# Kernel optimization log

Hardware: AMD Instinct MI355X
Metric: run time of the kernel (lower is better)

The kernel has to match this reference:

```python
import jax, jax.numpy as jnp
import numpy as np

N = 4096        # nodes
E = 131072      # edges (avg degree 32)
IN = 512        # in_channels
HID = 512       # hidden_channels
HEADS = 4       # GAT heads
LAYERS = 3      # residual GCN layers
G = 16          # graphs in batch
OUT = 1         # out_channels
NEG_SLOPE = 0.2 # GAT LeakyReLU slope


def setup_inputs() -> dict:
    key = jax.random.key(0)
    ks = jax.random.split(key, 9)
    s = 0.02
    x = jax.random.normal(ks[0], (N, IN), dtype=jnp.float32)
    edge_index = jax.random.randint(ks[1], (2, E), 0, N)
    batch = jnp.sort(jax.random.randint(ks[2], (N,), 0, G))
    W_gat = jax.random.normal(ks[3], (HEADS, IN, HID), dtype=jnp.float32) * s
    a_src = jax.random.normal(ks[4], (HEADS, HID), dtype=jnp.float32) * s
    a_dst = jax.random.normal(ks[5], (HEADS, HID), dtype=jnp.float32) * s
    W_gcn = jax.random.normal(ks[6], (LAYERS, HID, HID), dtype=jnp.float32) * s
    fc_w = jax.random.normal(ks[7], (HID, OUT), dtype=jnp.float32) * s
    fc_b = jnp.zeros((OUT,), dtype=jnp.float32)
    return {"x": x, "edge_index": edge_index, "batch": batch,
            "W_gat": W_gat, "a_src": a_src, "a_dst": a_dst,
            "W_gcn": W_gcn, "fc_w": fc_w, "fc_b": fc_b}


def reference(x, edge_index, batch, W_gat, a_src, a_dst, W_gcn, fc_w, fc_b):
    src, dst = edge_index[0], edge_index[1]

    # ---- LatentRelationCapturerGAT: multi-head GAT, one output per head ----
    h = jnp.einsum('nc,hcd->nhd', x, W_gat)                    # [N,H,D]
    lg_src = jnp.einsum('nhd,hd->nh', h, a_src)                # [N,H]
    lg_dst = jnp.einsum('nhd,hd->nh', h, a_dst)                # [N,H]
    e = jax.nn.leaky_relu(lg_src[src] + lg_dst[dst], NEG_SLOPE)  # [E,H]
    # segment softmax over incoming edges of each destination node
    m = jax.ops.segment_max(e, dst, num_segments=N)            # [N,H]
    w = jnp.exp(e - m[dst])                                    # [E,H]
    z = jax.ops.segment_sum(w, dst, num_segments=N)            # [N,H]
    alpha = w / (z[dst] + 1e-16)                               # [E,H]
    H0 = jax.ops.segment_sum(alpha[:, :, None] * h[src], dst, num_segments=N)  # [N,H,D]

    # ---- dense adjacency build + GCN normalization (shared across heads) ----
    A = jnp.zeros((N, N), dtype=x.dtype).at[src, dst].set(1.0)
    A = A + jnp.eye(N, dtype=x.dtype)                          # self-loops
    dinv = jax.lax.rsqrt(jnp.sum(A, axis=1))                   # deg >= 1
    A_hat = dinv[:, None] * A * dinv[None, :]                  # D^-1/2 (A+I) D^-1/2

    # ---- DeepResidualGCN: H <- relu(A_hat @ H @ W_l) + H (heads batched) ----
    H = H0
    for l in range(W_gcn.shape[0]):
        P = jnp.einsum('nm,mhd->nhd', A_hat, H)                # propagate
        H = jax.nn.relu(jnp.einsum('nhd,de->nhe', P, W_gcn[l])) + H

    # ---- per-head global mean pool, then mean over heads ----
    ones = jnp.ones((N,), dtype=x.dtype)
    cnt = jnp.maximum(jax.ops.segment_sum(ones, batch, num_segments=G), 1.0)  # [G]
    pooled = jax.ops.segment_sum(H, batch, num_segments=G) / cnt[:, None, None]  # [G,H,D]
    feats = pooled.mean(axis=1)                                # [G,D]

    return feats @ fc_w + fc_b                                 # [G,OUT]
```

## Files before the change

kernel.cpp:

```cpp
#include <hip/hip_runtime.h>
#include <cstdint>
#include <cstddef>

#define Nn    4096
#define Ee    131072
#define INC   512
#define HIDC  512
#define HEADS 4
#define NLAY  3
#define GG    16
#define FW    2048
#define ALDS  2112
#define BLDS  4160

typedef __attribute__((ext_vector_type(8))) short bfrag;
typedef __attribute__((ext_vector_type(4))) float ffrag;

__device__ __forceinline__ ushort f2bf(float v){
  uint u = __builtin_bit_cast(uint, v);
  u += 0x7fffu + ((u>>16)&1u);
  return (ushort)(u>>16);
}
__device__ __forceinline__ float bf2f(ushort s){
  uint u = ((uint)s)<<16; return __builtin_bit_cast(float, u);
}
__device__ __forceinline__ void fma8(float* acc, uint4 g, float w){
  uint u[4] = {g.x, g.y, g.z, g.w};
  #pragma unroll
  for (int q=0;q<4;q++){
    float lo = __builtin_bit_cast(float, u[q]<<16);
    float hi = __builtin_bit_cast(float, u[q] & 0xffff0000u);
    acc[2*q]   += w*lo;
    acc[2*q+1] += w*hi;
  }
}
__device__ __forceinline__ void pack8(void* p, const float* a){
  uint4 o;
  o.x = (uint)f2bf(a[0]) | ((uint)f2bf(a[1])<<16);
  o.y = (uint)f2bf(a[2]) | ((uint)f2bf(a[3])<<16);
  o.z = (uint)f2bf(a[4]) | ((uint)f2bf(a[5])<<16);
  o.w = (uint)f2bf(a[6]) | ((uint)f2bf(a[7])<<16);
  *(uint4*)p = o;
}

__global__ __launch_bounds__(256) void prep(
    const float* __restrict__ x, ushort* __restrict__ Xb,
    const float* __restrict__ Wgat, ushort* __restrict__ Tgat,
    const float* __restrict__ Wgcn, ushort* __restrict__ Tgcn,
    const int* __restrict__ src, const int* __restrict__ dst,
    int* __restrict__ indeg, unsigned int* __restrict__ bitmap,
    int* __restrict__ cnt_s, int* __restrict__ flag){
  __shared__ float tile[32][33];
  int b = blockIdx.x, t = threadIdx.x;
  if (b < 8192){
    int i = b*256 + t;
    Xb[i] = f2bf(x[i]);
  } else if (b < 9984){
    int idx = b - 8192;
    int z = idx >> 8, xy = idx & 255;
    const float* W; ushort* T; int bb;
    if (z < 4){ W = Wgat; T = Tgat; bb = z; } else { W = Wgcn; T = Tgcn; bb = z-4; }
    int r0 = (xy>>4)*32, c0 = (xy&15)*32;
    int i = t>>3, j0 = (t&7)*4;
    const float* Wb = W + (size_t)bb*512*512;
    float4 v = *(const float4*)(Wb + (size_t)(r0+i)*512 + c0 + j0);
    tile[i][j0]=v.x; tile[i][j0+1]=v.y; tile[i][j0+2]=v.z; tile[i][j0+3]=v.w;
    __syncthreads();
    ushort* o = T + (size_t)bb*512*512 + (size_t)(c0+i)*512 + r0 + j0;
    #pragma unroll
    for (int q=0;q<4;q++) o[q] = f2bf(tile[j0+q][i]);
  } else {
    int e = (b-9984)*256 + t; if (e>=Ee) return;
    int s = src[e], d = dst[e];
    atomicAdd(&indeg[d],1);
    unsigned int key = (unsigned int)s*Nn + (unsigned int)d;
    unsigned int bit = 1u<<(key&31);
    unsigned int old = atomicOr(&bitmap[key>>5], bit);
    int f = (old & bit) ? 0 : 1;
    flag[e] = f;
    if (f) atomicAdd(&cnt_s[s],1);
  }
}

__device__ __forceinline__ void gemm_core(
    const ushort* __restrict__ A, const ushort* __restrict__ B,
    const ushort* Res, ushort* Cb,
    int M, int N, int K, int relu_res, int m0, int n0,
    ushort* Ah, ushort* Bh)
{
  int t = threadIdx.x;
  int srA = t>>2, kqA = t&3;
  const ushort* pA = A + (size_t)(m0+srA)*K + kqA*8;
  int wA = (kqA*66 + srA)*8;
  int srB = t>>1, cB = t&1;
  const ushort* pB = B + (size_t)(n0+srB)*K + cB*16;
  int wB0 = ((2*cB)*130 + srB)*8;
  int wB1 = wB0 + 130*8;

  int wave = t>>6, lane = t&63;
  int wm = (wave&1)*32, wn = (wave>>1)*64;
  int lm = lane&15, quad = lane>>4;

  ffrag acc[2][4];
  #pragma unroll
  for (int i=0;i<2;i++){
    #pragma unroll
    for (int j=0;j<4;j++) acc[i][j] = (ffrag){0.f,0.f,0.f,0.f};
  }

  uint4 ra  = *(const uint4*)(pA);
  uint4 rb0 = *(const uint4*)(pB);  uint4 rb1 = *(const uint4*)(pB+8);
  *(uint4*)&Ah[wA]  = ra;
  *(uint4*)&Bh[wB0] = rb0; *(uint4*)&Bh[wB1] = rb1;
  if (K > 32){
    ra  = *(const uint4*)(pA+32);
    rb0 = *(const uint4*)(pB+32); rb1 = *(const uint4*)(pB+40);
  }
  __syncthreads();

  for (int k0 = 0; k0 < K; k0 += 32){
    int cur = (k0>>5)&1, nxt = cur^1;
    const ushort* Ac = Ah + cur*ALDS;
    const ushort* Bc = Bh + cur*BLDS;
    bfrag af[2];
    #pragma unroll
    for (int mt=0; mt<2; mt++)
      af[mt] = *(const bfrag*)&Ac[(quad*66 + wm + mt*16 + lm)*8];
    #pragma unroll
    for (int nt=0; nt<4; nt++){
      bfrag bf = *(const bfrag*)&Bc[(quad*130 + wn + nt*16 + lm)*8];
      #pragma unroll
      for (int mt=0; mt<2; mt++)
        acc[mt][nt] = __builtin_amdgcn_mfma_f32_16x16x32_bf16(af[mt], bf, acc[mt][nt], 0,0,0);
    }
    if (k0+32 < K){
      *(uint4*)&Ah[nxt*ALDS + wA]  = ra;
      *(uint4*)&Bh[nxt*BLDS + wB0] = rb0; *(uint4*)&Bh[nxt*BLDS + wB1] = rb1;
      if (k0+64 < K){
        ra  = *(const uint4*)(pA+k0+64);
        rb0 = *(const uint4*)(pB+k0+64); rb1 = *(const uint4*)(pB+k0+72);
      }
    }
    __syncthreads();
  }

  #pragma unroll
  for (int mt=0; mt<2; mt++){
    #pragma unroll
    for (int nt=0; nt<4; nt++){
      #pragma unroll
      for (int r=0;r<4;r++){
        int grow = m0 + wm + mt*16 + quad*4 + r;
        int gcol = n0 + wn + nt*16 + lm;
        size_t off = (size_t)grow*N + gcol;
        float v = acc[mt][nt][r];
        if (relu_res) v = fmaxf(v,0.f) + bf2f(Res[off]);
        Cb[off] = f2bf(v);
      }
    }
  }
}

__global__ __launch_bounds__(256) void gemm_bf(
    const ushort* __restrict__ A, const ushort* __restrict__ B,
    const ushort* Res, ushort* Cb,
    int M, int N, int K, int relu_res)
{
  __shared__ __align__(16) ushort Ah[2*ALDS];
  __shared__ __align__(16) ushort Bh[2*BLDS];
  gemm_core(A, B, Res, Cb, M, N, K, relu_res, blockIdx.y*64, blockIdx.x*128, Ah, Bh);
}

__global__ __launch_bounds__(256) void gat_gemm_ep2(
    const ushort* __restrict__ Xbf, const ushort* __restrict__ WgatT, ushort* __restrict__ hbf,
    const int* __restrict__ src, const int* __restrict__ dst, const int* __restrict__ flag,
    const int* __restrict__ rp_d, int* __restrict__ fill_d, int* __restrict__ slist,
    const int* __restrict__ rp_s, int* __restrict__ fill_s, int2* __restrict__ cw,
    const float* __restrict__ dinv)
{
  __shared__ __align__(16) ushort Ah[2*ALDS];
  __shared__ __align__(16) ushort Bh[2*BLDS];
  int b = blockIdx.x;
  if (b < 1024){
    int m0 = (b>>4)*64, n0 = (b&15)*128;
    gemm_core(Xbf, WgatT, nullptr, hbf, Nn, FW, INC, 0, m0, n0, Ah, Bh);
  } else {
    int e = (b-1024)*256 + threadIdx.x; if (e>=Ee) return;
    int s = src[e], d = dst[e];
    int p = atomicAdd(&fill_d[d],1); slist[rp_d[d]+p] = s;
    if (flag[e]){
      int q = atomicAdd(&fill_s[s],1);
      cw[rp_s[s]+q] = make_int2(d, __float_as_int(dinv[d]));
    }
  }
}

__global__ __launch_bounds__(256) void compute_lg(const ushort* __restrict__ hbf,
    const float* __restrict__ a_src, const float* __restrict__ a_dst,
    float* __restrict__ lgs, float* __restrict__ lgd){
  int n = blockIdx.x; int t = threadIdx.x;
  int hd = t>>6, lane = t&63;
  uint4 g = *(const uint4*)(hbf + (size_t)n*FW + hd*HIDC + lane*8);
  float h[8] = {0,0,0,0,0,0,0,0};
  fma8(h, g, 1.0f);
  float4 as0 = *(const float4*)(a_src + hd*HIDC + lane*8);
  float4 as1 = *(const float4*)(a_src + hd*HIDC + lane*8 + 4);
  float4 ad0 = *(const float4*)(a_dst + hd*HIDC + lane*8);
  float4 ad1 = *(const float4*)(a_dst + hd*HIDC + lane*8 + 4);
  float s1 = h[0]*as0.x + h[1]*as0.y + h[2]*as0.z + h[3]*as0.w
           + h[4]*as1.x + h[5]*as1.y + h[6]*as1.z + h[7]*as1.w;
  float s2 = h[0]*ad0.x + h[1]*ad0.y + h[2]*ad0.z + h[3]*ad0.w
           + h[4]*ad1.x + h[5]*ad1.y + h[6]*ad1.z + h[7]*ad1.w;
  for (int off=32; off; off>>=1){ s1 += __shfl_down(s1,off); s2 += __shfl_down(s2,off); }
  if (lane==0){ lgs[n*HEADS+hd]=s1; lgd[n*HEADS+hd]=s2; }
}

__global__ __launch_bounds__(1024) void scan3(const int* __restrict__ indeg, int* __restrict__ rp_d,
    const int* __restrict__ cnt_s, int* __restrict__ rp_s, float* __restrict__ dinv,
    const int* __restrict__ batch, int* __restrict__ goff){
  __shared__ int sums[1024];
  __shared__ int cnt2[GG];
  int t = threadIdx.x;
  if (blockIdx.x == 2){
    if (t<GG) cnt2[t]=0;
    __syncthreads();
    for (int i=t;i<Nn;i+=1024) atomicAdd(&cnt2[batch[i]],1);
    __syncthreads();
    if (t==0){ int run=0; for (int g=0; g<GG; g++){ goff[g]=run; run+=cnt2[g]; } goff[GG]=run; }
    return;
  }
  const int* cnt = blockIdx.x ? cnt_s : indeg;
  int* rowptr    = blockIdx.x ? rp_s  : rp_d;
  int v[4]; int s=0;
  #pragma unroll
  for (int i=0;i<4;i++){ int idx=t*4+i; v[i] = cnt[idx]; s+=v[i]; }
  sums[t]=s; __syncthreads();
  for (int off=1; off<1024; off<<=1){
    int other = (t>=off)? sums[t-off] : 0;
    __syncthreads();
    sums[t] += other;
    __syncthreads();
  }
  int run = (t>0)? sums[t-1] : 0;
  #pragma unroll
  for (int i=0;i<4;i++){
    int idx=t*4+i; rowptr[idx]=run; run+=v[i];
    if (blockIdx.x) dinv[idx] = 1.0f/sqrtf((float)(1+v[i]));
  }
  if (t==1023) rowptr[Nn]=sums[1023];
}

__global__ __launch_bounds__(256) void gat_aggregate(const ushort* __restrict__ hbf,
    const float* __restrict__ lgs, const float* __restrict__ lgd,
    const int* __restrict__ rowptr, const int* __restrict__ slist,
    ushort* __restrict__ Hbf){
  int t = threadIdx.x;
  int wv = __builtin_amdgcn_readfirstlane(t>>6);
  int lane = t&63;
  int b = blockIdx.x;
  int hd = __builtin_amdgcn_readfirstlane(b & 3);
  int n = ((b>>2)<<2) + wv;
  int beg = __builtin_amdgcn_readfirstlane(rowptr[n]);
  int end = __builtin_amdgcn_readfirstlane(rowptr[n+1]);
  int deg = end - beg;
  float ldst = lgd[n*HEADS+hd];
  float m_ = -3.4e38f, z_ = 0.f;
  for (int i=lane; i<deg; i+=64){
    int s = slist[beg+i];
    float v = lgs[s*HEADS+hd] + ldst;
    v = v>0.f ? v : 0.2f*v;
    float mn = fmaxf(m_, v);
    z_ = z_*__expf(m_-mn) + __expf(v-mn);
    m_ = mn;
  }
  for (int o=32;o;o>>=1){
    float mo = __shfl_down(m_,o), zo = __shfl_down(z_,o);
    float mn = fmaxf(m_, mo);
    z_ = z_*__expf(m_-mn) + zo*__expf(mo-mn);
    m_ = mn;
  }
  float mx = __shfl(m_,0);
  float zs = __shfl(z_,0);
  float inv = 1.f/(zs+1e-16f);
  float acc[8] = {0,0,0,0,0,0,0,0};
  const ushort* hb = hbf + hd*HIDC + lane*8;
  int i = beg;
  if (i+4 <= end){
    uint4 g0[4]; float lv0[4];
    #pragma unroll
    for (int q=0;q<4;q++){
      int s = slist[i+q];
      g0[q] = *(const uint4*)(hb + (size_t)s*FW);
      lv0[q] = lgs[s*HEADS+hd];
    }
    i += 4;
    for (; i+4<=end; i+=4){
      uint4 g1[4]; float lv1[4];
      #pragma unroll
      for (int q=0;q<4;q++){
        int s = slist[i+q];
        g1[q] = *(const uint4*)(hb + (size_t)s*FW);
        lv1[q] = lgs[s*HEADS+hd];
      }
      #pragma unroll
      for (int q=0;q<4;q++){
        float v = lv0[q] + ldst; v = v>0.f ? v : 0.2f*v;
        fma8(acc, g0[q], __expf(v-mx)*inv);
      }
      #pragma unroll
      for (int q=0;q<4;q++){ g0[q]=g1[q]; lv0[q]=lv1[q]; }
    }
    #pragma unroll
    for (int q=0;q<4;q++){
      float v = lv0[q] + ldst; v = v>0.f ? v : 0.2f*v;
      fma8(acc, g0[q], __expf(v-mx)*inv);
    }
  }
  for (; i<end; i++){
    int s = slist[i];
    uint4 g = *(const uint4*)(hb + (size_t)s*FW);
    float v = lgs[s*HEADS+hd] + ldst; v = v>0.f ? v : 0.2f*v;
    fma8(acc, g, __expf(v-mx)*inv);
  }
  size_t off = (size_t)n*FW + hd*HIDC + lane*8;
  pack8(Hbf + off, acc);
}

__global__ __launch_bounds__(256) void spmm_bf(const ushort* __restrict__ Hbf,
    ushort* __restrict__ Phi,
    const int* __restrict__ rowptr, const int2* __restrict__ cw, const float* __restrict__ dinv){
  int t = threadIdx.x;
  int wv = __builtin_amdgcn_readfirstlane(t>>6);
  int lane = t&63;
  int b = blockIdx.x;
  int ck = __builtin_amdgcn_readfirstlane(b & 3);
  int n = ((b>>2)<<2) + wv;
  int f = (ck<<9) + lane*8;
  float di = dinv[n];
  float acc[8] = {0,0,0,0,0,0,0,0};
  const ushort* hb = Hbf + f;
  uint4 self = *(const uint4*)(hb + (size_t)n*FW);
  fma8(acc, self, di*di);
  int beg = __builtin_amdgcn_readfirstlane(rowptr[n]);
  int end = __builtin_amdgcn_readfirstlane(rowptr[n+1]);
  int i = beg;
  if (i+4 <= end){
    int2 e0[4]; uint4 g0[4];
    #pragma unroll
    for (int q=0;q<4;q++) e0[q] = cw[i+q];
    #pragma unroll
    for (int q=0;q<4;q++) g0[q] = *(const uint4*)(hb + (size_t)e0[q].x*FW);
    i += 4;
    for (; i+4<=end; i+=4){
      int2 e1[4]; uint4 g1[4];
      #pragma unroll
      for (int q=0;q<4;q++) e1[q] = cw[i+q];
      #pragma unroll
      for (int q=0;q<4;q++) g1[q] = *(const uint4*)(hb + (size_t)e1[q].x*FW);
      #pragma unroll
      for (int q=0;q<4;q++) fma8(acc, g0[q], di*__int_as_float(e0[q].y));
      #pragma unroll
      for (int q=0;q<4;q++){ e0[q]=e1[q]; g0[q]=g1[q]; }
    }
    #pragma unroll
    for (int q=0;q<4;q++) fma8(acc, g0[q], di*__int_as_float(e0[q].y));
  }
  for (; i<end; i++){
    int2 e = cw[i];
    uint4 g = *(const uint4*)(hb + (size_t)e.x*FW);
    fma8(acc, g, di*__int_as_float(e.y));
  }
  pack8(Phi + (size_t)n*FW + f, acc);
}

__global__ __launch_bounds__(256) void pool_accum(const ushort* __restrict__ Hb,
    const int* __restrict__ batch, float* __restrict__ psum){
  int d2 = blockIdx.y*256 + threadIdx.x;
  int n0 = blockIdx.x*32;
  int g = batch[n0];
  float s0 = 0.f, s1 = 0.f;
  for (int k=0;k<32;k++){
    int n = n0+k;
    int gn = batch[n];
    if (gn != g){
      atomicAdd(&psum[(size_t)g*FW + d2*2],   s0);
      atomicAdd(&psum[(size_t)g*FW + d2*2+1], s1);
      s0=0.f; s1=0.f; g=gn;
    }
    uint v = *(const uint*)(Hb + (size_t)n*FW + d2*2);
    s0 += bf2f((ushort)(v&0xffff));
    s1 += bf2f((ushort)(v>>16));
  }
  atomicAdd(&psum[(size_t)g*FW + d2*2],   s0);
  atomicAdd(&psum[(size_t)g*FW + d2*2+1], s1);
}
__global__ __launch_bounds__(256) void final_out(const float* __restrict__ psum,
    const int* __restrict__ goff,
    const float* __restrict__ fc_w, const float* __restrict__ fc_b, float* __restrict__ out){
  int g = blockIdx.x; int t = threadIdx.x;
  float cinv = 0.25f / fmaxf((float)(goff[g+1]-goff[g]), 1.f);
  float p = 0.f;
  for (int d=t; d<HIDC; d+=256){
    float f = cinv*(psum[(size_t)g*FW+d] + psum[(size_t)g*FW+HIDC+d]
                  + psum[(size_t)g*FW+2*HIDC+d] + psum[(size_t)g*FW+3*HIDC+d]);
    p += f*fc_w[d];
  }
  __shared__ float red[4];
  for (int off=32; off; off>>=1) p += __shfl_down(p,off);
  if ((t&63)==0) red[t>>6]=p;
  __syncthreads();
  if (t==0) out[g] = red[0]+red[1]+red[2]+red[3] + fc_b[0];
}

extern "C" void kernel_launch(void* const* d_in, const int* in_sizes, int n_in,
                              void* d_out, int out_size, void* d_ws, size_t ws_size,
                              hipStream_t stream){
  const float* x      = (const float*)d_in[0];
  const int*   ei     = (const int*)d_in[1];
  const int*   batch  = (const int*)d_in[2];
  const float* W_gat  = (const float*)d_in[3];
  const float* a_src  = (const float*)d_in[4];
  const float* a_dst  = (const float*)d_in[5];
  const float* W_gcn  = (const float*)d_in[6];
  const float* fc_w   = (const float*)d_in[7];
  const float* fc_b   = (const float*)d_in[8];
  float* out = (float*)d_out;
  const int* src = ei;
  const int* dst = ei + Ee;

  char* w = (char*)d_ws;
  size_t off = 0;
  auto alloc = [&](size_t bytes)->char*{ char* p = w + off; off = (off + bytes + 255) & ~(size_t)255; return p; };
  ushort* hbf    = (ushort*)alloc((size_t)Nn*FW*2);
  ushort* Hbf    = (ushort*)alloc((size_t)Nn*FW*2);
  ushort* Xbf    = (ushort*)alloc((size_t)Nn*INC*2);
  ushort* WgatT  = (ushort*)alloc((size_t)HEADS*INC*HIDC*2);
  ushort* WgcnT  = (ushort*)alloc((size_t)NLAY*HIDC*HIDC*2);
  float* lgs    = (float*)alloc((size_t)Nn*HEADS*4);
  float* lgd    = (float*)alloc((size_t)Nn*HEADS*4);
  int* indeg    = (int*)alloc(Nn*4);
  int* fill_d   = (int*)alloc(Nn*4);
  int* cnt_s    = (int*)alloc(Nn*4);
  int* fill_s   = (int*)alloc(Nn*4);
  float* psum   = (float*)alloc((size_t)GG*FW*4);
  unsigned int* bitmap = (unsigned int*)alloc((size_t)Nn*Nn/8);
  size_t zero_bytes = (size_t)Nn*4*4 + (size_t)GG*FW*4 + (size_t)Nn*Nn/8;
  int* rowptr_d = (int*)alloc((Nn+1)*4);
  int* slist    = (int*)alloc(Ee*4);
  int* rowptr_s = (int*)alloc((Nn+1)*4);
  int2* cwlist  = (int2*)alloc((size_t)Ee*8);
  int* flag     = (int*)alloc(Ee*4);
  float* dinv   = (float*)alloc(Nn*4);
  int* goff     = (int*)alloc((GG+1)*4);
  ushort* Phi   = hbf;

  hipMemsetAsync(indeg, 0, zero_bytes, stream);

  prep<<<10496,256,0,stream>>>(x, Xbf, W_gat, WgatT, W_gcn, WgcnT,
                               src, dst, indeg, bitmap, cnt_s, flag);

  scan3<<<3,1024,0,stream>>>(indeg, rowptr_d, cnt_s, rowptr_s, dinv, batch, goff);

  gat_gemm_ep2<<<1536,256,0,stream>>>(Xbf, WgatT, hbf,
      src, dst, flag, rowptr_d, fill_d, slist, rowptr_s, fill_s, cwlist, dinv);

  compute_lg<<<Nn,256,0,stream>>>(hbf, a_src, a_dst, lgs, lgd);
  gat_aggregate<<<Nn,256,0,stream>>>(hbf, lgs, lgd, rowptr_d, slist, Hbf);

  for (int l=0;l<NLAY;l++){
    spmm_bf<<<Nn,256,0,stream>>>(Hbf, Phi, rowptr_s, cwlist, dinv);
    gemm_bf<<<dim3(HIDC/128, (Nn*HEADS)/64),256,0,stream>>>(Phi,
        WgcnT + (size_t)l*HIDC*HIDC,
        Hbf, Hbf, Nn*HEADS, HIDC, HIDC, 1);
  }

  pool_accum<<<dim3(Nn/32, FW/512),256,0,stream>>>(Hbf, batch, psum);
  final_out<<<GG,256,0,stream>>>(psum, goff, fc_w, fc_b, out);
}
```

Measured before the change: 361.5 us.

## Fuse x bf16 conversion into GAT GEMM loads and attention logits into epilogue

```diff
diff --git a/kernel.cpp b/kernel.cpp
--- a/kernel.cpp
+++ b/kernel.cpp
@@ -42,9 +42,16 @@
   o.w = (uint)f2bf(a[6]) | ((uint)f2bf(a[7])<<16);
   *(uint4*)p = o;
 }
+__device__ __forceinline__ uint4 cvt8(float4 a, float4 b){
+  uint4 o;
+  o.x = (uint)f2bf(a.x) | ((uint)f2bf(a.y)<<16);
+  o.y = (uint)f2bf(a.z) | ((uint)f2bf(a.w)<<16);
+  o.z = (uint)f2bf(b.x) | ((uint)f2bf(b.y)<<16);
+  o.w = (uint)f2bf(b.z) | ((uint)f2bf(b.w)<<16);
+  return o;
+}
 
 __global__ __launch_bounds__(256) void prep(
-    const float* __restrict__ x, ushort* __restrict__ Xb,
     const float* __restrict__ Wgat, ushort* __restrict__ Tgat,
     const float* __restrict__ Wgcn, ushort* __restrict__ Tgcn,
     const int* __restrict__ src, const int* __restrict__ dst,
@@ -52,12 +59,8 @@
     int* __restrict__ cnt_s, int* __restrict__ flag){
   __shared__ float tile[32][33];
   int b = blockIdx.x, t = threadIdx.x;
-  if (b < 8192){
-    int i = b*256 + t;
-    Xb[i] = f2bf(x[i]);
-  } else if (b < 9984){
-    int idx = b - 8192;
-    int z = idx >> 8, xy = idx & 255;
+  if (b < 1792){
+    int z = b >> 8, xy = b & 255;
     const float* W; ushort* T; int bb;
     if (z < 4){ W = Wgat; T = Tgat; bb = z; } else { W = Wgcn; T = Tgcn; bb = z-4; }
     int r0 = (xy>>4)*32, c0 = (xy&15)*32;
@@ -70,7 +73,7 @@
     #pragma unroll
     for (int q=0;q<4;q++) o[q] = f2bf(tile[j0+q][i]);
   } else {
-    int e = (b-9984)*256 + t; if (e>=Ee) return;
+    int e = (b-1792)*256 + t; if (e>=Ee) return;
     int s = src[e], d = dst[e];
     atomicAdd(&indeg[d],1);
     unsigned int key = (unsigned int)s*Nn + (unsigned int)d;
@@ -82,15 +85,17 @@
   }
 }
 
+template<bool AF32, bool FUSELG>
 __device__ __forceinline__ void gemm_core(
-    const ushort* __restrict__ A, const ushort* __restrict__ B,
+    const void* __restrict__ Av, const ushort* __restrict__ B,
     const ushort* Res, ushort* Cb,
-    int M, int N, int K, int relu_res, int m0, int n0,
-    ushort* Ah, ushort* Bh)
+    int N, int K, int relu_res, int m0, int n0,
+    ushort* Ah, ushort* Bh,
+    const float* a_src, const float* a_dst, float* lgs, float* lgd)
 {
+  __shared__ float lsum[64][2];
   int t = threadIdx.x;
   int srA = t>>2, kqA = t&3;
-  const ushort* pA = A + (size_t)(m0+srA)*K + kqA*8;
   int wA = (kqA*66 + srA)*8;
   int srB = t>>1, cB = t&1;
   const ushort* pB = B + (size_t)(n0+srB)*K + cB*16;
@@ -101,6 +106,10 @@
   int wm = (wave&1)*32, wn = (wave>>1)*64;
   int lm = lane&15, quad = lane>>4;
 
+  if (FUSELG){
+    if (t < 128) lsum[t>>1][t&1] = 0.f;
+  }
+
   ffrag acc[2][4];
   #pragma unroll
   for (int i=0;i<2;i++){
@@ -108,12 +117,18 @@
     for (int j=0;j<4;j++) acc[i][j] = (ffrag){0.f,0.f,0.f,0.f};
   }
 
-  uint4 ra  = *(const uint4*)(pA);
+  const ushort* pA16 = (const ushort*)Av + (size_t)(m0+srA)*K + kqA*8;
+  const float*  pA32 = (const float*)Av  + (size_t)(m0+srA)*K + kqA*8;
+
+  uint4 ra; float4 raf0, raf1;
+  if (AF32){ raf0 = *(const float4*)(pA32); raf1 = *(const float4*)(pA32+4); }
+  else     { ra = *(const uint4*)(pA16); }
   uint4 rb0 = *(const uint4*)(pB);  uint4 rb1 = *(const uint4*)(pB+8);
-  *(uint4*)&Ah[wA]  = ra;
+  *(uint4*)&Ah[wA]  = AF32 ? cvt8(raf0, raf1) : ra;
   *(uint4*)&Bh[wB0] = rb0; *(uint4*)&Bh[wB1] = rb1;
   if (K > 32){
-    ra  = *(const uint4*)(pA+32);
+    if (AF32){ raf0 = *(const float4*)(pA32+32); raf1 = *(const float4*)(pA32+36); }
+    else     { ra = *(const uint4*)(pA16+32); }
     rb0 = *(const uint4*)(pB+32); rb1 = *(const uint4*)(pB+40);
   }
   __syncthreads();
@@ -134,29 +149,53 @@
         acc[mt][nt] = __builtin_amdgcn_mfma_f32_16x16x32_bf16(af[mt], bf, acc[mt][nt], 0,0,0);
     }
     if (k0+32 < K){
-      *(uint4*)&Ah[nxt*ALDS + wA]  = ra;
+      *(uint4*)&Ah[nxt*ALDS + wA]  = AF32 ? cvt8(raf0, raf1) : ra;
       *(uint4*)&Bh[nxt*BLDS + wB0] = rb0; *(uint4*)&Bh[nxt*BLDS + wB1] = rb1;
       if (k0+64 < K){
-        ra  = *(const uint4*)(pA+k0+64);
+        if (AF32){ raf0 = *(const float4*)(pA32+k0+64); raf1 = *(const float4*)(pA32+k0+68); }
+        else     { ra = *(const uint4*)(pA16+k0+64); }
         rb0 = *(const uint4*)(pB+k0+64); rb1 = *(const uint4*)(pB+k0+72);
       }
     }
     __syncthreads();
   }
 
+  float asv[4], adv[4];
+  if (FUSELG){
+    #pragma unroll
+    for (int nt=0;nt<4;nt++){
+      int gcol = n0 + wn + nt*16 + lm;
+      asv[nt] = a_src[gcol]; adv[nt] = a_dst[gcol];
+    }
+  }
   #pragma unroll
   for (int mt=0; mt<2; mt++){
     #pragma unroll
-    for (int nt=0; nt<4; nt++){
-      #pragma unroll
-      for (int r=0;r<4;r++){
-        int grow = m0 + wm + mt*16 + quad*4 + r;
+    for (int r=0;r<4;r++){
+      int row = wm + mt*16 + quad*4 + r;
+      int grow = m0 + row;
+      float p1 = 0.f, p2 = 0.f;
+      #pragma unroll
+      for (int nt=0; nt<4; nt++){
         int gcol = n0 + wn + nt*16 + lm;
         size_t off = (size_t)grow*N + gcol;
         float v = acc[mt][nt][r];
         if (relu_res) v = fmaxf(v,0.f) + bf2f(Res[off]);
         Cb[off] = f2bf(v);
+        if (FUSELG){ p1 += v*asv[nt]; p2 += v*adv[nt]; }
       }
+      if (FUSELG){
+        atomicAdd(&lsum[row][0], p1);
+        atomicAdd(&lsum[row][1], p2);
+      }
+    }
+  }
+  if (FUSELG){
+    __syncthreads();
+    if (t < 64){
+      int hd = n0 >> 9;
+      atomicAdd(&lgs[(size_t)(m0+t)*HEADS + hd], lsum[t][0]);
+      atomicAdd(&lgd[(size_t)(m0+t)*HEADS + hd], lsum[t][1]);
     }
   }
 }
@@ -164,15 +203,19 @@
 __global__ __launch_bounds__(256) void gemm_bf(
     const ushort* __restrict__ A, const ushort* __restrict__ B,
     const ushort* Res, ushort* Cb,
-    int M, int N, int K, int relu_res)
+    int N, int K, int relu_res)
 {
   __shared__ __align__(16) ushort Ah[2*ALDS];
   __shared__ __align__(16) ushort Bh[2*BLDS];
-  gemm_core(A, B, Res, Cb, M, N, K, relu_res, blockIdx.y*64, blockIdx.x*128, Ah, Bh);
+  gemm_core<false,false>(A, B, Res, Cb, N, K, relu_res,
+                         blockIdx.y*64, blockIdx.x*128, Ah, Bh,
+                         nullptr, nullptr, nullptr, nullptr);
 }
 
 __global__ __launch_bounds__(256) void gat_gemm_ep2(
-    const ushort* __restrict__ Xbf, const ushort* __restrict__ WgatT, ushort* __restrict__ hbf,
+    const float* __restrict__ x, const ushort* __restrict__ WgatT, ushort* __restrict__ hbf,
+    const float* __restrict__ a_src, const float* __restrict__ a_dst,
+    float* __restrict__ lgs, float* __restrict__ lgd,
     const int* __restrict__ src, const int* __restrict__ dst, const int* __restrict__ flag,
     const int* __restrict__ rp_d, int* __restrict__ fill_d, int* __restrict__ slist,
     const int* __restrict__ rp_s, int* __restrict__ fill_s, int2* __restrict__ cw,
@@ -183,7 +226,8 @@
   int b = blockIdx.x;
   if (b < 1024){
     int m0 = (b>>4)*64, n0 = (b&15)*128;
-    gemm_core(Xbf, WgatT, nullptr, hbf, Nn, FW, INC, 0, m0, n0, Ah, Bh);
+    gemm_core<true,true>(x, WgatT, nullptr, hbf, FW, INC, 0, m0, n0, Ah, Bh,
+                         a_src, a_dst, lgs, lgd);
   } else {
     int e = (b-1024)*256 + threadIdx.x; if (e>=Ee) return;
     int s = src[e], d = dst[e];
@@ -193,26 +237,6 @@
       cw[rp_s[s]+q] = make_int2(d, __float_as_int(dinv[d]));
     }
   }
-}
-
-__global__ __launch_bounds__(256) void compute_lg(const ushort* __restrict__ hbf,
-    const float* __restrict__ a_src, const float* __restrict__ a_dst,
-    float* __restrict__ lgs, float* __restrict__ lgd){
-  int n = blockIdx.x; int t = threadIdx.x;
-  int hd = t>>6, lane = t&63;
-  uint4 g = *(const uint4*)(hbf + (size_t)n*FW + hd*HIDC + lane*8);
-  float h[8] = {0,0,0,0,0,0,0,0};
-  fma8(h, g, 1.0f);
-  float4 as0 = *(const float4*)(a_src + hd*HIDC + lane*8);
-  float4 as1 = *(const float4*)(a_src + hd*HIDC + lane*8 + 4);
-  float4 ad0 = *(const float4*)(a_dst + hd*HIDC + lane*8);
-  float4 ad1 = *(const float4*)(a_dst + hd*HIDC + lane*8 + 4);
-  float s1 = h[0]*as0.x + h[1]*as0.y + h[2]*as0.z + h[3]*as0.w
-           + h[4]*as1.x + h[5]*as1.y + h[6]*as1.z + h[7]*as1.w;
-  float s2 = h[0]*ad0.x + h[1]*ad0.y + h[2]*ad0.z + h[3]*ad0.w
-           + h[4]*ad1.x + h[5]*ad1.y + h[6]*ad1.z + h[7]*ad1.w;
-  for (int off=32; off; off>>=1){ s1 += __shfl_down(s1,off); s2 += __shfl_down(s2,off); }
-  if (lane==0){ lgs[n*HEADS+hd]=s1; lgd[n*HEADS+hd]=s2; }
 }
 
 __global__ __launch_bounds__(1024) void scan3(const int* __restrict__ indeg, int* __restrict__ rp_d,
@@ -433,18 +457,17 @@
   auto alloc = [&](size_t bytes)->char*{ char* p = w + off; off = (off + bytes + 255) & ~(size_t)255; return p; };
   ushort* hbf    = (ushort*)alloc((size_t)Nn*FW*2);
   ushort* Hbf    = (ushort*)alloc((size_t)Nn*FW*2);
-  ushort* Xbf    = (ushort*)alloc((size_t)Nn*INC*2);
   ushort* WgatT  = (ushort*)alloc((size_t)HEADS*INC*HIDC*2);
   ushort* WgcnT  = (ushort*)alloc((size_t)NLAY*HIDC*HIDC*2);
-  float* lgs    = (float*)alloc((size_t)Nn*HEADS*4);
-  float* lgd    = (float*)alloc((size_t)Nn*HEADS*4);
   int* indeg    = (int*)alloc(Nn*4);
   int* fill_d   = (int*)alloc(Nn*4);
   int* cnt_s    = (int*)alloc(Nn*4);
   int* fill_s   = (int*)alloc(Nn*4);
   float* psum   = (float*)alloc((size_t)GG*FW*4);
+  float* lgs    = (float*)alloc((size_t)Nn*HEADS*4);
+  float* lgd    = (float*)alloc((size_t)Nn*HEADS*4);
   unsigned int* bitmap = (unsigned int*)alloc((size_t)Nn*Nn/8);
-  size_t zero_bytes = (size_t)Nn*4*4 + (size_t)GG*FW*4 + (size_t)Nn*Nn/8;
+  size_t zero_bytes = (size_t)Nn*4*4 + (size_t)GG*FW*4 + (size_t)Nn*HEADS*4*2 + (size_t)Nn*Nn/8;
   int* rowptr_d = (int*)alloc((Nn+1)*4);
   int* slist    = (int*)alloc(Ee*4);
   int* rowptr_s = (int*)alloc((Nn+1)*4);
@@ -456,22 +479,21 @@
 
   hipMemsetAsync(indeg, 0, zero_bytes, stream);
 
-  prep<<<10496,256,0,stream>>>(x, Xbf, W_gat, WgatT, W_gcn, WgcnT,
-                               src, dst, indeg, bitmap, cnt_s, flag);
+  prep<<<2304,256,0,stream>>>(W_gat, WgatT, W_gcn, WgcnT,
+                              src, dst, indeg, bitmap, cnt_s, flag);
 
   scan3<<<3,1024,0,stream>>>(indeg, rowptr_d, cnt_s, rowptr_s, dinv, batch, goff);
 
-  gat_gemm_ep2<<<1536,256,0,stream>>>(Xbf, WgatT, hbf,
+  gat_gemm_ep2<<<1536,256,0,stream>>>(x, WgatT, hbf, a_src, a_dst, lgs, lgd,
       src, dst, flag, rowptr_d, fill_d, slist, rowptr_s, fill_s, cwlist, dinv);
 
-  compute_lg<<<Nn,256,0,stream>>>(hbf, a_src, a_dst, lgs, lgd);
   gat_aggregate<<<Nn,256,0,stream>>>(hbf, lgs, lgd, rowptr_d, slist, Hbf);
 
   for (int l=0;l<NLAY;l++){
     spmm_bf<<<Nn,256,0,stream>>>(Hbf, Phi, rowptr_s, cwlist, dinv);
     gemm_bf<<<dim3(HIDC/128, (Nn*HEADS)/64),256,0,stream>>>(Phi,
         WgcnT + (size_t)l*HIDC*HIDC,
-        Hbf, Hbf, Nn*HEADS, HIDC, HIDC, 1);
+        Hbf, Hbf, HIDC, HIDC, 1);
   }
 
   pool_accum<<<dim3(Nn/32, FW/512),256,0,stream>>>(Hbf, batch, psum);
```

After: 372.4 us. +3.0%, slower.
